# Optimization experiments

Hardware: AMD Instinct MI355X
Metric: run time of the kernel (lower is better)

The kernel has to match this reference:

```python
import jax, jax.numpy as jnp
import numpy as np

EPS = 1e-8
PAD = 1  # kernel // 2 for kernel=3


def setup_inputs() -> dict:
    key = jax.random.key(0)
    k1, k2, k3, k4, k5 = jax.random.split(key, 5)
    b, c, h, w = 16, 256, 64, 64
    out_ch, kernel, style_dim = 256, 3, 512
    x = jax.random.normal(k1, (b, c, h, w), dtype=jnp.float32)
    style = jax.random.normal(k2, (b, style_dim), dtype=jnp.float32)
    # learned params
    weight = jax.random.normal(k3, (1, out_ch, c, kernel, kernel), dtype=jnp.float32)
    lim = 1.0 / np.sqrt(style_dim)
    mod_w = jax.random.uniform(k4, (c, style_dim), minval=-lim, maxval=lim, dtype=jnp.float32)
    mod_b = jax.random.uniform(k5, (c,), minval=-lim, maxval=lim, dtype=jnp.float32)
    return {"x": x, "style": style, "weight": weight, "mod_w": mod_w, "mod_b": mod_b}


def reference(x, style, weight, mod_w, mod_b):
    # s[b,i]: per-sample, per-input-channel modulation from the style Linear
    s = style @ mod_w.T + mod_b                     # [b, in_ch]
    w = weight[0]                                    # [out_ch, in_ch, k, k]
    # demod factor: sum_{i,kh,kw} (w[o,i,kh,kw]*s[b,i])^2 = sum_i s^2 * sum_kk w^2
    w_sq = jnp.sum(w * w, axis=(2, 3))               # [out_ch, in_ch]
    d = jax.lax.rsqrt(jnp.einsum('oi,bi->bo', w_sq, s * s) + EPS)  # [b, out_ch]
    # modulate input channels instead of materializing per-sample weights
    xs = x * s[:, :, None, None]                     # [b, in_ch, h, w]
    y = jax.lax.conv_general_dilated(
        xs, w, window_strides=(1, 1), padding=[(PAD, PAD), (PAD, PAD)],
        dimension_numbers=('NCHW', 'OIHW', 'NCHW'))
    return y * d[:, :, None, None]                   # [b, out_ch, h, w]
```

## Files before the change

### kernel.cpp

```cpp
#include <hip/hip_runtime.h>
#include <hip/hip_bf16.h>
#include <cstdint>
#include <cstddef>

typedef __bf16 bf16_t;
typedef __bf16 bf16x8 __attribute__((ext_vector_type(8)));
typedef float  f32x4  __attribute__((ext_vector_type(4)));

#define NB   16
#define NC   256
#define NO   256
#define SD   512
#define NPIX 4096
#define CELL 40

#define WS_S   0
#define WS_D   16384
#define WS_WSQ 32768
#define WS_WT  294912

__global__ __launch_bounds__(256) void prep1(
    const float* __restrict__ style, const float* __restrict__ weight,
    const float* __restrict__ mod_w, const float* __restrict__ mod_b,
    float* __restrict__ s_buf, float* __restrict__ wsqT, bf16_t* __restrict__ wT)
{
    const int blk = blockIdx.x;
    const int tid = threadIdx.x;
    if (blk < 16) {
        const int b = blk, i = tid;
        const float* st = style + b * SD;
        const float* mw = mod_w + i * SD;
        float acc = 0.f;
        for (int k = 0; k < SD; k += 4) {
            float4 a = *(const float4*)(st + k);
            float4 c = *(const float4*)(mw + k);
            acc += a.x * c.x + a.y * c.y + a.z * c.z + a.w * c.w;
        }
        s_buf[b * NC + i] = acc + mod_b[i];
    } else {
        const int o = blk - 16, i = tid;
        const float* wp = weight + (o * NC + i) * 9;
        const int qi = (i >> 3) & 3;
        const int f  = (o >> 1) & 3;
        const int ci = (i & ~31) | (((qi + f) & 3) << 3) | (i & 7);
        float q = 0.f;
        #pragma unroll
        for (int t = 0; t < 9; ++t) {
            float v = wp[t];
            q += v * v;
            wT[t * (NO * NC) + o * NC + ci] = (bf16_t)v;
        }
        wsqT[i * NO + o] = q;
    }
}

__global__ __launch_bounds__(256) void prep2(
    const float* __restrict__ s_buf, const float* __restrict__ wsqT,
    float* __restrict__ d_buf)
{
    __shared__ float sh[NC];
    const int b = blockIdx.x, o = threadIdx.x;
    float sv = s_buf[b * NC + o];
    sh[o] = sv * sv;
    __syncthreads();
    float sum = 0.f;
    for (int i = 0; i < NC; ++i)
        sum += wsqT[i * NO + o] * sh[i];
    d_buf[b * NC + o] = rsqrtf(sum + 1e-8f);
}

__device__ __forceinline__ void stage_a(const bf16_t* __restrict__ wT_tap,
                                        int o0, int ic0, bf16_t* dst, int tid)
{
    #pragma unroll
    for (int it = 0; it < 2; ++it) {
        int s = it * 256 + tid;
        const bf16_t* g = wT_tap + (o0 + (s >> 2)) * NC + ic0 + (s & 3) * 8;
        __builtin_amdgcn_global_load_lds(
            (const __attribute__((address_space(1))) void*)g,
            (__attribute__((address_space(3))) void*)(dst + s * 8),
            16, 0, 0);
    }
}

__global__ __launch_bounds__(256) void conv_mfma(
    const float* __restrict__ x,
    const bf16_t* __restrict__ wT,
    const float* __restrict__ s_buf,
    const float* __restrict__ d_buf,
    float* __restrict__ out)
{
    __shared__ bf16_t lds_a[2][128 * 32];
    __shared__ bf16_t lds_b[4 * 64 * CELL];

    const int tid   = threadIdx.x;
    const int lane  = tid & 63;
    const int wv    = tid >> 6;
    const int wo    = wv >> 1;
    const int wp    = wv & 1;
    const int pt    = blockIdx.x;
    const int o0    = blockIdx.y * 128;
    const int batch = blockIdx.z;
    const int row0  = pt * 2;

    const int l15 = lane & 15;
    const int q   = lane >> 4;
    const int sAo = ((q + ((l15 >> 1) & 3)) & 3) * 8;

    const int colB = tid & 63;
    const int cgrp = tid >> 6;

    f32x4 acc[4][4];
    #pragma unroll
    for (int i = 0; i < 4; ++i)
        #pragma unroll
        for (int j = 0; j < 4; ++j) {
            f32x4 z = {0.f, 0.f, 0.f, 0.f};
            acc[i][j] = z;
        }

    bf16x8 bzero;
    #pragma unroll
    for (int j = 0; j < 8; ++j) bzero[j] = (bf16_t)0.f;

    for (int chunk = 0; chunk < 8; ++chunk) {
        const int ic0 = chunk * 32;

        {
            float sv[8];
            #pragma unroll
            for (int c = 0; c < 8; ++c)
                sv[c] = s_buf[batch * NC + ic0 + cgrp * 8 + c];
            const float* xb = x + (size_t)(batch * NC + ic0 + cgrp * 8) * NPIX + colB;
            #pragma unroll
            for (int r = 0; r < 4; ++r) {
                const int gy = row0 - 1 + r;
                const bool valid = ((unsigned)gy < 64u);
                bf16x8 pk;
                #pragma unroll
                for (int cp = 0; cp < 4; ++cp) {
                    float v0 = 0.f, v1 = 0.f;
                    if (valid) {
                        v0 = xb[(2 * cp)     * NPIX + gy * 64] * sv[2 * cp];
                        v1 = xb[(2 * cp + 1) * NPIX + gy * 64] * sv[2 * cp + 1];
                    }
                    pk[2 * cp]     = (bf16_t)v0;
                    pk[2 * cp + 1] = (bf16_t)v1;
                }
                *(bf16x8*)&lds_b[(r * 64 + colB) * CELL + cgrp * 8] = pk;
            }
        }
        stage_a(wT, o0, ic0, &lds_a[0][0], tid);
        __syncthreads();

        #pragma unroll
        for (int tap = 0; tap < 9; ++tap) {
            if (tap < 8)
                stage_a(wT + (tap + 1) * (NO * NC), o0, ic0,
                        &lds_a[(tap + 1) & 1][0], tid);

            const bf16_t* abuf = &lds_a[tap & 1][0];
            const int kh = tap / 3, kw = tap % 3;

            bf16x8 af[4];
            #pragma unroll
            for (int of = 0; of < 4; ++of)
                af[of] = *(const bf16x8*)&abuf[(wo * 64 + of * 16 + l15) * 32 + sAo];

            const int r = wp + kh;
            #pragma unroll
            for (int nf = 0; nf < 4; ++nf) {
                const int c = nf * 16 + l15 + kw - 1;
                bf16x8 bfr;
                if ((unsigned)c < 64u) {
                    bfr = *(const bf16x8*)&lds_b[(r * 64 + c) * CELL + q * 8];
                } else {
                    bfr = bzero;
                }
                #pragma unroll
                for (int of = 0; of < 4; ++of)
                    acc[of][nf] = __builtin_amdgcn_mfma_f32_16x16x32_bf16(
                        af[of], bfr, acc[of][nf], 0, 0, 0);
            }
            __syncthreads();
        }
    }

    const int p_base = pt * 128 + wp * 64;
    #pragma unroll
    for (int of = 0; of < 4; ++of) {
        #pragma unroll
        for (int rg = 0; rg < 4; ++rg) {
            const int o_g = o0 + wo * 64 + of * 16 + q * 4 + rg;
            const float dv = d_buf[batch * NO + o_g];
            const size_t obase = (size_t)(batch * NO + o_g) * NPIX;
            #pragma unroll
            for (int nf = 0; nf < 4; ++nf) {
                const int p_g = p_base + nf * 16 + l15;
                out[obase + p_g] = acc[of][nf][rg] * dv;
            }
        }
    }
}

extern "C" void kernel_launch(void* const* d_in, const int* in_sizes, int n_in,
                              void* d_out, int out_size, void* d_ws, size_t ws_size,
                              hipStream_t stream)
{
    const float* x      = (const float*)d_in[0];
    const float* style  = (const float*)d_in[1];
    const float* weight = (const float*)d_in[2];
    const float* mod_w  = (const float*)d_in[3];
    const float* mod_b  = (const float*)d_in[4];
    float* out = (float*)d_out;

    char* ws = (char*)d_ws;
    float*  s_buf = (float*)(ws + WS_S);
    float*  d_buf = (float*)(ws + WS_D);
    float*  wsqT  = (float*)(ws + WS_WSQ);
    bf16_t* wT    = (bf16_t*)(ws + WS_WT);

    hipLaunchKernelGGL(prep1, dim3(272), dim3(256), 0, stream,
                       style, weight, mod_w, mod_b, s_buf, wsqT, wT);
    hipLaunchKernelGGL(prep2, dim3(16), dim3(256), 0, stream, s_buf, wsqT, d_buf);
    hipLaunchKernelGGL(conv_mfma, dim3(32, 2, 16), dim3(256), 0, stream,
                       x, wT, s_buf, d_buf, out);
}
```

Before: 286.5 us.

## Load weight fragments directly from global into registers, pad LDS halo columns

Weight tiles are no longer staged through double-buffered LDS with per-tap barriers. Each wave now loads its A fragments straight from global (L2-resident) memory into registers, prefetching the next tap while the current one computes. The B tile gets zeroed halo columns so the boundary branch goes away, and the per-tap __syncthreads is reduced to one per chunk. A launch-bounds occupancy hint of 4 blocks is added. The cost is redundant global loads of weights across waves and more register pressure.

```diff
diff --git a/kernel.cpp b/kernel.cpp
--- a/kernel.cpp
+++ b/kernel.cpp
@@ -7,12 +7,13 @@
 typedef __bf16 bf16x8 __attribute__((ext_vector_type(8)));
 typedef float  f32x4  __attribute__((ext_vector_type(4)));
 
-#define NB   16
-#define NC   256
-#define NO   256
-#define SD   512
-#define NPIX 4096
-#define CELL 40
+#define NB    16
+#define NC    256
+#define NO    256
+#define SD    512
+#define NPIX  4096
+#define CELL  40
+#define BCOLS 66
 
 #define WS_S   0
 #define WS_D   16384
@@ -40,15 +41,12 @@
     } else {
         const int o = blk - 16, i = tid;
         const float* wp = weight + (o * NC + i) * 9;
-        const int qi = (i >> 3) & 3;
-        const int f  = (o >> 1) & 3;
-        const int ci = (i & ~31) | (((qi + f) & 3) << 3) | (i & 7);
         float q = 0.f;
         #pragma unroll
         for (int t = 0; t < 9; ++t) {
             float v = wp[t];
             q += v * v;
-            wT[t * (NO * NC) + o * NC + ci] = (bf16_t)v;
+            wT[t * (NO * NC) + o * NC + i] = (bf16_t)v;
         }
         wsqT[i * NO + o] = q;
     }
@@ -69,29 +67,14 @@
     d_buf[b * NC + o] = rsqrtf(sum + 1e-8f);
 }
 
-__device__ __forceinline__ void stage_a(const bf16_t* __restrict__ wT_tap,
-                                        int o0, int ic0, bf16_t* dst, int tid)
-{
-    #pragma unroll
-    for (int it = 0; it < 2; ++it) {
-        int s = it * 256 + tid;
-        const bf16_t* g = wT_tap + (o0 + (s >> 2)) * NC + ic0 + (s & 3) * 8;
-        __builtin_amdgcn_global_load_lds(
-            (const __attribute__((address_space(1))) void*)g,
-            (__attribute__((address_space(3))) void*)(dst + s * 8),
-            16, 0, 0);
-    }
-}
-
-__global__ __launch_bounds__(256) void conv_mfma(
+__global__ __launch_bounds__(256, 4) void conv_mfma(
     const float* __restrict__ x,
     const bf16_t* __restrict__ wT,
     const float* __restrict__ s_buf,
     const float* __restrict__ d_buf,
     float* __restrict__ out)
 {
-    __shared__ bf16_t lds_a[2][128 * 32];
-    __shared__ bf16_t lds_b[4 * 64 * CELL];
+    __shared__ bf16_t lds_b[4 * BCOLS * CELL];
 
     const int tid   = threadIdx.x;
     const int lane  = tid & 63;
@@ -105,10 +88,20 @@
 
     const int l15 = lane & 15;
     const int q   = lane >> 4;
-    const int sAo = ((q + ((l15 >> 1) & 3)) & 3) * 8;
 
     const int colB = tid & 63;
     const int cgrp = tid >> 6;
+
+    const bf16_t* pA = wT + (size_t)(o0 + wo * 64 + l15) * NC + q * 8;
+
+    if (tid < 32) {
+        const int gr = tid >> 3, side = (tid >> 2) & 1, slot = tid & 3;
+        const int col = side ? 65 : 0;
+        bf16x8 z;
+        #pragma unroll
+        for (int j = 0; j < 8; ++j) z[j] = (bf16_t)0.f;
+        *(bf16x8*)&lds_b[(gr * BCOLS + col) * CELL + slot * 8] = z;
+    }
 
     f32x4 acc[4][4];
     #pragma unroll
@@ -118,10 +111,6 @@
             f32x4 z = {0.f, 0.f, 0.f, 0.f};
             acc[i][j] = z;
         }
-
-    bf16x8 bzero;
-    #pragma unroll
-    for (int j = 0; j < 8; ++j) bzero[j] = (bf16_t)0.f;
 
     for (int chunk = 0; chunk < 8; ++chunk) {
         const int ic0 = chunk * 32;
@@ -147,43 +136,44 @@
                     pk[2 * cp]     = (bf16_t)v0;
                     pk[2 * cp + 1] = (bf16_t)v1;
                 }
-                *(bf16x8*)&lds_b[(r * 64 + colB) * CELL + cgrp * 8] = pk;
-            }
-        }
-        stage_a(wT, o0, ic0, &lds_a[0][0], tid);
+                *(bf16x8*)&lds_b[(r * BCOLS + colB + 1) * CELL + cgrp * 8] = pk;
+            }
+        }
         __syncthreads();
 
+        const bf16_t* pAc = pA + ic0;
+
+        bf16x8 afn[4];
+        #pragma unroll
+        for (int of = 0; of < 4; ++of)
+            afn[of] = *(const bf16x8*)(pAc + of * 16 * NC);
+
         #pragma unroll
         for (int tap = 0; tap < 9; ++tap) {
-            if (tap < 8)
-                stage_a(wT + (tap + 1) * (NO * NC), o0, ic0,
-                        &lds_a[(tap + 1) & 1][0], tid);
-
-            const bf16_t* abuf = &lds_a[tap & 1][0];
+            bf16x8 afc[4];
+            #pragma unroll
+            for (int of = 0; of < 4; ++of) afc[of] = afn[of];
+
+            if (tap < 8) {
+                #pragma unroll
+                for (int of = 0; of < 4; ++of)
+                    afn[of] = *(const bf16x8*)(pAc + (size_t)(tap + 1) * NO * NC
+                                               + of * 16 * NC);
+            }
+
             const int kh = tap / 3, kw = tap % 3;
-
-            bf16x8 af[4];
-            #pragma unroll
-            for (int of = 0; of < 4; ++of)
-                af[of] = *(const bf16x8*)&abuf[(wo * 64 + of * 16 + l15) * 32 + sAo];
-
-            const int r = wp + kh;
+            const int r  = wp + kh;
             #pragma unroll
             for (int nf = 0; nf < 4; ++nf) {
-                const int c = nf * 16 + l15 + kw - 1;
-                bf16x8 bfr;
-                if ((unsigned)c < 64u) {
-                    bfr = *(const bf16x8*)&lds_b[(r * 64 + c) * CELL + q * 8];
-                } else {
-                    bfr = bzero;
-                }
+                const int c = nf * 16 + l15 + kw;
+                bf16x8 bfr = *(const bf16x8*)&lds_b[(r * BCOLS + c) * CELL + q * 8];
                 #pragma unroll
                 for (int of = 0; of < 4; ++of)
                     acc[of][nf] = __builtin_amdgcn_mfma_f32_16x16x32_bf16(
-                        af[of], bfr, acc[of][nf], 0, 0, 0);
-            }
-            __syncthreads();
-        }
+                        afc[of], bfr, acc[of][nf], 0, 0, 0);
+            }
+        }
+        __syncthreads();
     }
 
     const int p_base = pt * 128 + wp * 64;
```

After: 290.0 us. Within noise of the previous version (+1.2%).
